# Kernel optimization log

Measured on AMD Instinct MI355X. Metric: run time of the kernel, lower is better.

Reference implementation:

```python
import jax, jax.numpy as jnp
import numpy as np
from jax import lax

NQ = 9          # num_qubits
K = 3           # basis_size
S = 16          # max_num_snapshots
H = 128         # hidden_size
B = 16          # batch
D = 2 ** NQ

# basis_reconstruction buffer = Pauli X, Y, Z (complex64), non-trainable
PAULI = jnp.array([[[0, 1], [1, 0]],
                   [[0, -1j], [1j, 0]],
                   [[1, 0], [0, -1]]], dtype=jnp.complex64)


def setup_inputs() -> dict:
    key = jax.random.key(0)
    ks = jax.random.split(key, 11)
    return {
        "snapshot": jax.random.normal(ks[0], (B, NQ), jnp.float32),
        "basis_comp_vector": jax.random.uniform(ks[1], (B, NQ, K), dtype=jnp.float32),
        "rho": jax.random.normal(ks[2], (B, 2) + (2,) * NQ, jnp.float32),
        "h0": jax.random.normal(ks[3], (B, H), jnp.float32),
        "c0": jax.random.normal(ks[4], (B, H), jnp.float32),
        "W_ih": jax.random.normal(ks[5], (4 * H, NQ + NQ * K), jnp.float32) * 0.1,
        "W_hh": jax.random.normal(ks[6], (4 * H, H), jnp.float32) * 0.1,
        "b_ih": jax.random.normal(ks[7], (4 * H,), jnp.float32) * 0.1,
        "b_hh": jax.random.normal(ks[8], (4 * H,), jnp.float32) * 0.1,
        "Wp": jax.random.normal(ks[9], (NQ, K, H), jnp.float32) * 0.1,
        "bp": jax.random.normal(ks[10], (NQ, K), jnp.float32) * 0.1,
    }


def _lstm_cell(x, h, c, W_ih, W_hh, b_ih, b_hh):
    g = x @ W_ih.T + h @ W_hh.T + b_ih + b_hh
    i, f, gg, o = jnp.split(g, 4, axis=-1)  # torch gate order i,f,g,o
    i, f, o = jax.nn.sigmoid(i), jax.nn.sigmoid(f), jax.nn.sigmoid(o)
    c = f * c + i * jnp.tanh(gg)
    return o * jnp.tanh(c), c


def _apply_1q(psi, M, i):
    """Apply per-batch 2x2 matrix M [B,2,2] to qubit i of psi [B]+[2]*NQ."""
    psi = jnp.moveaxis(psi, 1 + i, 1)
    sh = psi.shape
    out = jnp.einsum('bij,bjr->bir', M, psi.reshape(sh[0], 2, -1))
    return jnp.moveaxis(out.reshape(sh), 1, 1 + i)


def _take_snapshots(psi, a):
    """Vectorized take_snapshot: psi [B]+[2]*NQ complex, a [B,NQ,K] real (sqrt of probs).
    For each qubit build psi_plus/psi_minus projectors, record expectation
    s = <P+> - <P-> and collapse onto the (normalized) plus branch."""
    axs = tuple(range(1, NQ + 1))
    zeros = jnp.zeros(psi.shape[0], jnp.float32)
    ss = []
    for i in range(NQ):
        a1, a2, a3 = a[:, i, 0], a[:, i, 1], a[:, i, 2]
        an = jnp.sqrt(a1 * a1 + a2 * a2 + a3 * a3)
        nrm = 1.0 / jnp.sqrt(2.0 * an * (a3 + an))
        pp = jnp.stack([lax.complex(a3 + an, zeros), lax.complex(a1, a2)], axis=-1) * nrm[:, None]
        pm = jnp.stack([lax.complex(-a1, a2), lax.complex(a3 + an, zeros)], axis=-1) * nrm[:, None]
        Pp = pp[:, :, None] * jnp.conj(pp)[:, None, :]  # [B,2,2]
        Pm = pm[:, :, None] * jnp.conj(pm)[:, None, :]
        psi_p = _apply_1q(psi, Pp, i)
        psi_m = _apply_1q(psi, Pm, i)
        prob_p = jnp.sum(psi_p.real ** 2 + psi_p.imag ** 2, axis=axs)
        prob_m = jnp.sum(psi_m.real ** 2 + psi_m.imag ** 2, axis=axs)
        ss.append(prob_p - prob_m)
        psi = psi_p / jnp.sqrt(prob_p).reshape((-1,) + (1,) * NQ)  # collapse
    return jnp.stack(ss, axis=1)  # [B,NQ]


def _bkron(A, Bm):
    b, m, n = A.shape
    p, q = Bm.shape[1], Bm.shape[2]
    return (A[:, :, None, :, None] * Bm[:, None, :, None, :]).reshape(b, m * p, n * q)


def _forward(snapshot, basis_comp_vector, rho, h0, c0, W_ih, W_hh, b_ih, b_hh, Wp, bp):
    b = snapshot.shape[0]
    psi = lax.complex(rho[:, 0], rho[:, 1])  # [B]+[2]*NQ pure state
    x = jnp.concatenate([snapshot, basis_comp_vector.reshape(b, -1)], axis=-1)
    inputs = [x]
    h, c = h0, c0
    for _ in range(S - 1):
        h, c = _lstm_cell(x, h, c, W_ih, W_hh, b_ih, b_hh)
        probs = jax.nn.softmax(jnp.einsum('bh,nkh->bnk', h, Wp) + bp, axis=-1)
        amps = jnp.sqrt(probs)  # [B,NQ,K]
        snap = _take_snapshots(psi, amps)
        x = jnp.concatenate([snap, amps.reshape(b, -1)], axis=-1)
        inputs.append(x)
    # classical-shadow reconstruction, summed over snapshots
    I2 = jnp.eye(2, dtype=jnp.complex64)
    acc = jnp.zeros((b, D, D), jnp.complex64)
    last_bv = None
    for x in inputs:
        shadow = x[:, :NQ]                                   # [B,NQ]
        bv = x[:, NQ:].reshape(b, NQ, K)
        last_bv = bv
        basis = jnp.einsum('bnk,kij->bnij', bv.astype(jnp.complex64), PAULI)
        rho_q = (I2 + shadow[:, :, None, None].astype(jnp.complex64) * basis * 3.0) / 2.0
        r = rho_q[:, 0]
        for iq in range(1, NQ):
            r = _bkron(r, rho_q[:, iq])
        acc = acc + r
    rho_rec = acc / S
    out = jnp.stack([rho_rec.real, rho_rec.imag], axis=1)  # [B,2,D,D]
    return out, last_bv


def reference(snapshot, basis_comp_vector, rho, h0, c0, W_ih, W_hh, b_ih, b_hh, Wp, bp):
    return _forward(snapshot, basis_comp_vector, rho, h0, c0,
                    W_ih, W_hh, b_ih, b_hh, Wp, bp)
```

## Files before the change

kernel.cpp:

```cpp
#include <hip/hip_runtime.h>
#include <math.h>

#define NQ 9
#define KK 3
#define S 16
#define H 128
#define BB 16
#define D 512
#define DD (D*D)

__device__ __forceinline__ float sigf(float x){ return 1.f/(1.f + __expf(-x)); }

#define DPP_ADD(x, ctrl, rmask) \
  x += __int_as_float(__builtin_amdgcn_update_dpp(0, __float_as_int(x), ctrl, rmask, 0xf, false))

__device__ __forceinline__ float wave_red_sum(float x) {
  DPP_ADD(x, 0x111, 0xf);
  DPP_ADD(x, 0x112, 0xf);
  DPP_ADD(x, 0x114, 0xf);
  DPP_ADD(x, 0x118, 0xf);
  DPP_ADD(x, 0x142, 0xa);
  DPP_ADD(x, 0x143, 0xc);
  return __int_as_float(__builtin_amdgcn_readlane(__float_as_int(x), 63));
}
#define RL(v, l) __int_as_float(__builtin_amdgcn_readlane(__float_as_int(v), (l)))
#define DPP_ROR(x, n) \
  __int_as_float(__builtin_amdgcn_update_dpp(0, __float_as_int(x), 0x120 + (n), 0xf, 0xf, false))

__global__ __launch_bounds__(512, 2)
void seq_kernel(const float* __restrict__ snapshot,
                const float* __restrict__ bcv,
                const float* __restrict__ rho,
                const float* __restrict__ h0,
                const float* __restrict__ c0,
                const float* __restrict__ W_ih,
                const float* __restrict__ W_hh,
                const float* __restrict__ b_ih,
                const float* __restrict__ b_hh,
                const float* __restrict__ Wp,
                const float* __restrict__ bp,
                float4* __restrict__ mats,
                float* __restrict__ last_bv)
{
  const int b    = blockIdx.x;
  const int tid  = threadIdx.x;
  const int lane = tid & 63;
  const int w    = tid >> 6;

  __shared__ __align__(16) float xh[164];
  __shared__ float gbuf[512];
  __shared__ float prj[27];

  float4 wih[9], whh[32];
  {
    const float4* wi = (const float4*)(W_ih + tid*36);
    #pragma unroll
    for (int k = 0; k < 9; ++k) wih[k] = wi[k];
    const float4* wh = (const float4*)(W_hh + tid*H);
    #pragma unroll
    for (int k = 0; k < 32; ++k) whh[k] = wh[k];
  }
  const float bias = b_ih[tid] + b_hh[tid];
  float2 wpv[4]; float bpv[4];
  #pragma unroll
  for (int i = 0; i < 4; ++i) {
    int u = w + 8*i;
    if (u < 27) { wpv[i] = *(const float2*)(Wp + u*H + 2*lane); bpv[i] = bp[u]; }
    else        { wpv[i] = make_float2(0.f, 0.f); bpv[i] = 0.f; }
  }

  float cc0 = c0[b*H + 2*lane], cc1 = c0[b*H + 2*lane + 1];

  float pr0[8], pi0[8], norm0 = 0.f;
  if (w == 0) {
    #pragma unroll
    for (int j = 0; j < 8; ++j) {
      pr0[j] = rho[b*1024 + j*64 + lane];
      pi0[j] = rho[b*1024 + 512 + j*64 + lane];
    }
    float ls = 0.f;
    #pragma unroll
    for (int j = 0; j < 8; ++j) ls += pr0[j]*pr0[j] + pi0[j]*pi0[j];
    norm0 = wave_red_sum(ls);
  }

  if (tid < 128) xh[36 + tid] = h0[b*H + tid];
  if (tid < NQ)  xh[tid]      = snapshot[b*NQ + tid];
  if (tid < 27)  xh[NQ + tid] = bcv[b*27 + tid];
  __syncthreads();

  if (tid < NQ) {
    float s = xh[tid], v0 = xh[9+tid*3], v1 = xh[9+tid*3+1], v2 = xh[9+tid*3+2];
    mats[(b*S + 0)*NQ + tid] = make_float4(
        0.5f*(1.f + 3.f*s*v2), 1.5f*s*v0, -1.5f*s*v1, 0.5f*(1.f - 3.f*s*v2));
  }

  for (int t = 1; t < S; ++t) {
    {
      const float4* x4 = (const float4*)xh;
      float g0 = bias, g1 = 0.f, g2 = 0.f, g3 = 0.f;
      #pragma unroll
      for (int k = 0; k < 9; ++k) {
        float4 wv = wih[k], xv = x4[k];
        g0 += wv.x*xv.x; g1 += wv.y*xv.y; g2 += wv.z*xv.z; g3 += wv.w*xv.w;
      }
      #pragma unroll
      for (int k = 0; k < 32; ++k) {
        float4 wv = whh[k], xv = x4[9 + k];
        g0 += wv.x*xv.x; g1 += wv.y*xv.y; g2 += wv.z*xv.z; g3 += wv.w*xv.w;
      }
      gbuf[tid] = (g0 + g1) + (g2 + g3);
    }
    __syncthreads();

    float h0v, h1v;
    {
      float2 gI = *(const float2*)(gbuf + 2*lane);
      float2 gF = *(const float2*)(gbuf + 128 + 2*lane);
      float2 gG = *(const float2*)(gbuf + 256 + 2*lane);
      float2 gO = *(const float2*)(gbuf + 384 + 2*lane);
      cc0 = sigf(gF.x)*cc0 + sigf(gI.x)*tanhf(gG.x);
      cc1 = sigf(gF.y)*cc1 + sigf(gI.y)*tanhf(gG.y);
      h0v = sigf(gO.x)*tanhf(cc0);
      h1v = sigf(gO.y)*tanhf(cc1);
    }
    if (w == 1) *(float2*)(xh + 36 + 2*lane) = make_float2(h0v, h1v);

    #pragma unroll
    for (int i = 0; i < 4; ++i) {
      float p = wave_red_sum(wpv[i].x*h0v + wpv[i].y*h1v);
      int u = w + 8*i;
      if (u < 27 && lane == 0) prj[u] = p + bpv[i];
    }
    __syncthreads();

    if (w == 0) {
      float a1 = 0.f, a2 = 0.f, a3 = 0.f;
      float k0v = 0.f, k1rv = 0.f, k1iv = 0.f;
      if (lane < NQ) {
        float l0 = prj[lane*3], l1 = prj[lane*3+1], l2 = prj[lane*3+2];
        float mx = fmaxf(l0, fmaxf(l1, l2));
        float e0 = __expf(l0 - mx), e1 = __expf(l1 - mx), e2 = __expf(l2 - mx);
        float inv = 1.f/(e0 + e1 + e2);
        a1 = sqrtf(e0*inv); a2 = sqrtf(e1*inv); a3 = sqrtf(e2*inv);
        float an = sqrtf(a1*a1 + a2*a2 + a3*a3);
        float t3 = a3 + an;
        float n1 = 1.f/sqrtf(2.f*an*t3);
        k0v = n1*t3; k1rv = n1*a1; k1iv = -n1*a2;
      }
      float part[9];

      float r4[4], i4[4];
      {
        const float K0 = RL(k0v,0), K1r = RL(k1rv,0), K1i = RL(k1iv,0);
        float lp = 0.f;
        #pragma unroll
        for (int j = 0; j < 4; ++j) {
          r4[j] = K0*pr0[j] + K1r*pr0[j+4] - K1i*pi0[j+4];
          i4[j] = K0*pi0[j] + K1r*pi0[j+4] + K1i*pr0[j+4];
          lp += r4[j]*r4[j] + i4[j]*i4[j];
        }
        part[0] = lp;
      }
      float r2[2], i2[2];
      {
        const float K0 = RL(k0v,1), K1r = RL(k1rv,1), K1i = RL(k1iv,1);
        float lp = 0.f;
        #pragma unroll
        for (int j = 0; j < 2; ++j) {
          r2[j] = K0*r4[j] + K1r*r4[j+2] - K1i*i4[j+2];
          i2[j] = K0*i4[j] + K1r*i4[j+2] + K1i*r4[j+2];
          lp += r2[j]*r2[j] + i2[j]*i2[j];
        }
        part[1] = lp;
      }
      float wr, wi_;
      {
        const float K0 = RL(k0v,2), K1r = RL(k1rv,2), K1i = RL(k1iv,2);
        wr  = K0*r2[0] + K1r*r2[1] - K1i*i2[1];
        wi_ = K0*i2[0] + K1r*i2[1] + K1i*r2[1];
        part[2] = wr*wr + wi_*wi_;
      }
      #pragma unroll
      for (int q = 3; q < 5; ++q) {
        const int half = 32 >> (q - 3);
        const float K0 = RL(k0v,q), K1r = RL(k1rv,q), K1i = RL(k1iv,q);
        float pr = __shfl(wr,  lane + half, 64);
        float pi = __shfl(wi_, lane + half, 64);
        float nr = K0*wr  + K1r*pr - K1i*pi;
        float ni = K0*wi_ + K1r*pi + K1i*pr;
        wr = nr; wi_ = ni;
        part[q] = (lane < half) ? (nr*nr + ni*ni) : 0.f;
      }
      #pragma unroll
      for (int q = 5; q < NQ; ++q) {
        const int half = 32 >> (q - 3);
        const float K0 = RL(k0v,q), K1r = RL(k1rv,q), K1i = RL(k1iv,q);
        float pr, pi;
        if      (q == 5) { pr = DPP_ROR(wr, 8);  pi = DPP_ROR(wi_, 8);  }
        else if (q == 6) { pr = DPP_ROR(wr, 12); pi = DPP_ROR(wi_, 12); }
        else if (q == 7) { pr = DPP_ROR(wr, 14); pi = DPP_ROR(wi_, 14); }
        else             { pr = DPP_ROR(wr, 15); pi = DPP_ROR(wi_, 15); }
        float nr = K0*wr  + K1r*pr - K1i*pi;
        float ni = K0*wi_ + K1r*pi + K1i*pr;
        wr = nr; wi_ = ni;
        part[q] = (lane < half) ? (nr*nr + ni*ni) : 0.f;
      }
      float L[9];
      #pragma unroll
      for (int q = 0; q < NQ; ++q) L[q] = wave_red_sum(part[q]);
      float sv = 2.f*L[0] - norm0;
      #pragma unroll
      for (int q = 1; q < NQ; ++q) {
        float r = 2.f*L[q]/L[q-1] - 1.f;
        sv = (lane == q) ? r : sv;
      }
      if (lane < NQ) {
        xh[lane] = sv;
        xh[9 + lane*3]     = a1;
        xh[9 + lane*3 + 1] = a2;
        xh[9 + lane*3 + 2] = a3;
        mats[(b*S + t)*NQ + lane] = make_float4(
            0.5f*(1.f + 3.f*sv*a3), 1.5f*sv*a1,
            -1.5f*sv*a2,            0.5f*(1.f - 3.f*sv*a3));
      }
    }
    __syncthreads();
  }

  if (tid < 27) last_bv[b*27 + tid] = xh[9 + tid];
}

__device__ __forceinline__ void herm_entry(float4 m, int rb, int cb, float& er, float& ei) {
  if (rb == 0) { if (cb == 0) { er = m.x; ei = 0.f; } else { er = m.y; ei = m.z; } }
  else         { if (cb == 0) { er = m.y; ei = -m.z; } else { er = m.w; ei = 0.f; } }
}

__global__ __launch_bounds__(512, 2)
void kron_kernel(const float4* __restrict__ mats_g, float* __restrict__ out)
{
  const int b   = blockIdx.y;
  const int bm  = blockIdx.x;
  const int tid = threadIdx.x;
  const int rTp = bm >> 3;
  const int rg  = bm & 7;

  __shared__ float4 matsh[S*NQ];
  __shared__ float2 top[S][2][16];
  __shared__ __align__(16) float2 bot[4][S][32];

  if (tid < S*NQ) matsh[tid] = mats_g[b*S*NQ + tid];
  __syncthreads();

  {
    int t = tid >> 5, rTi = (tid >> 4) & 1, cT = tid & 15;
    int rT = rTp*2 + rTi;
    float re = 1.f, im = 0.f;
    #pragma unroll
    for (int q = 0; q < 4; ++q) {
      int rb = (rT >> (3 - q)) & 1, cb = (cT >> (3 - q)) & 1;
      float er, ei; herm_entry(matsh[t*NQ + q], rb, cb, er, ei);
      float nr = re*er - im*ei; im = re*ei + im*er; re = nr;
    }
    top[t][rTi][cT] = make_float2(re, im);
  }
  {
    int r_ = tid >> 7, t_ = (tid >> 3) & 15, cB0 = (tid & 7) << 2;
    int rB = rg*4 + r_;
    #pragma unroll
    for (int i = 0; i < 4; ++i) {
      int cB = cB0 + i;
      float re = 1.f, im = 0.f;
      #pragma unroll
      for (int q = 0; q < 5; ++q) {
        int rb = (rB >> (4 - q)) & 1, cb = (cB >> (4 - q)) & 1;
        float er, ei; herm_entry(matsh[t_*NQ + 4 + q], rb, cb, er, ei);
        float nr = re*er - im*ei; im = re*ei + im*er; re = nr;
      }
      bot[r_][t_][cB] = make_float2(re, im);
    }
  }
  __syncthreads();

  const int rb = tid >> 7;
  const int c0 = (tid & 127) << 2;
  const int cT = c0 >> 5, cB = c0 & 31;
  float4 a0r = make_float4(0,0,0,0), a0i = make_float4(0,0,0,0);
  float4 a1r = make_float4(0,0,0,0), a1i = make_float4(0,0,0,0);
  #pragma unroll
  for (int t = 0; t < S; ++t) {
    float4 b01 = *(const float4*)&bot[rb][t][cB];
    float4 b23 = *(const float4*)&bot[rb][t][cB + 2];
    float2 tA = top[t][0][cT];
    float2 tB = top[t][1][cT];
    a0r.x += tA.x*b01.x - tA.y*b01.y;  a0i.x += tA.x*b01.y + tA.y*b01.x;
    a0r.y += tA.x*b01.z - tA.y*b01.w;  a0i.y += tA.x*b01.w + tA.y*b01.z;
    a0r.z += tA.x*b23.x - tA.y*b23.y;  a0i.z += tA.x*b23.y + tA.y*b23.x;
    a0r.w += tA.x*b23.z - tA.y*b23.w;  a0i.w += tA.x*b23.w + tA.y*b23.z;
    a1r.x += tB.x*b01.x - tB.y*b01.y;  a1i.x += tB.x*b01.y + tB.y*b01.x;
    a1r.y += tB.x*b01.z - tB.y*b01.w;  a1i.y += tB.x*b01.w + tB.y*b01.z;
    a1r.z += tB.x*b23.x - tB.y*b23.y;  a1i.z += tB.x*b23.y + tB.y*b23.x;
    a1r.w += tB.x*b23.z - tB.y*b23.w;  a1i.w += tB.x*b23.w + tB.y*b23.z;
  }
  const float invS = 1.f/16.f;
  a0r.x*=invS; a0r.y*=invS; a0r.z*=invS; a0r.w*=invS;
  a0i.x*=invS; a0i.y*=invS; a0i.z*=invS; a0i.w*=invS;
  a1r.x*=invS; a1r.y*=invS; a1r.z*=invS; a1r.w*=invS;
  a1i.x*=invS; a1i.y*=invS; a1i.z*=invS; a1i.w*=invS;
  const int rowA = (rTp*2)*32 + rg*4 + rb;
  const int rowB = rowA + 32;
  size_t baseA = ((size_t)b*2)*DD + (size_t)rowA*D + c0;
  size_t baseB = ((size_t)b*2)*DD + (size_t)rowB*D + c0;
  *(float4*)(out + baseA)      = a0r;
  *(float4*)(out + baseA + DD) = a0i;
  *(float4*)(out + baseB)      = a1r;
  *(float4*)(out + baseB + DD) = a1i;
}

extern "C" void kernel_launch(void* const* d_in, const int* in_sizes, int n_in,
                              void* d_out, int out_size, void* d_ws, size_t ws_size,
                              hipStream_t stream) {
  const float* snapshot = (const float*)d_in[0];
  const float* bcv      = (const float*)d_in[1];
  const float* rho      = (const float*)d_in[2];
  const float* h0       = (const float*)d_in[3];
  const float* c0       = (const float*)d_in[4];
  const float* W_ih     = (const float*)d_in[5];
  const float* W_hh     = (const float*)d_in[6];
  const float* b_ih     = (const float*)d_in[7];
  const float* b_hh     = (const float*)d_in[8];
  const float* Wp       = (const float*)d_in[9];
  const float* bp       = (const float*)d_in[10];

  float*  out     = (float*)d_out;
  float4* mats    = (float4*)d_ws;
  float*  last_bv = out + (size_t)BB*2*DD;

  seq_kernel<<<BB, 512, 0, stream>>>(snapshot, bcv, rho, h0, c0,
                                     W_ih, W_hh, b_ih, b_hh, Wp, bp,
                                     mats, last_bv);

  dim3 grid(64, BB);
  kron_kernel<<<grid, 512, 0, stream>>>(mats, out);
}
```

Before: 171.5 us.

## Broadcast hidden state via lane reads and enlarge kron output tile per block

The LSTM recurrent matvec now takes h from registers through cross-lane reads (RL) instead of shared memory. It is computed right after the snapshot step, so one h store and its shared-memory round trip leave the critical path. The kron kernel now computes four top rows per block instead of two, halving the grid and reusing each bottom-factor load across more outputs. This raises register pressure in the kron kernel and reduces the number of blocks available to hide store latency.

```diff
diff --git a/kernel.cpp b/kernel.cpp
--- a/kernel.cpp
+++ b/kernel.cpp
@@ -47,7 +47,7 @@
   const int lane = tid & 63;
   const int w    = tid >> 6;
 
-  __shared__ __align__(16) float xh[164];
+  __shared__ __align__(16) float xh[36];
   __shared__ float gbuf[512];
   __shared__ float prj[27];
 
@@ -70,6 +70,7 @@
   }
 
   float cc0 = c0[b*H + 2*lane], cc1 = c0[b*H + 2*lane + 1];
+  float h0v = h0[b*H + 2*lane], h1v = h0[b*H + 2*lane + 1];
 
   float pr0[8], pi0[8], norm0 = 0.f;
   if (w == 0) {
@@ -84,36 +85,39 @@
     norm0 = wave_red_sum(ls);
   }
 
-  if (tid < 128) xh[36 + tid] = h0[b*H + tid];
   if (tid < NQ)  xh[tid]      = snapshot[b*NQ + tid];
   if (tid < 27)  xh[NQ + tid] = bcv[b*27 + tid];
-  __syncthreads();
-
   if (tid < NQ) {
-    float s = xh[tid], v0 = xh[9+tid*3], v1 = xh[9+tid*3+1], v2 = xh[9+tid*3+2];
+    float s  = snapshot[b*NQ + tid];
+    float v0 = bcv[b*27 + tid*3];
+    float v1 = bcv[b*27 + tid*3 + 1];
+    float v2 = bcv[b*27 + tid*3 + 2];
     mats[(b*S + 0)*NQ + tid] = make_float4(
         0.5f*(1.f + 3.f*s*v2), 1.5f*s*v0, -1.5f*s*v1, 0.5f*(1.f - 3.f*s*v2));
   }
+
+  float ghh = bias;
+  #pragma unroll
+  for (int j = 0; j < 32; ++j) {
+    float4 wv = whh[j];
+    ghh += wv.x*RL(h0v, 2*j)     + wv.y*RL(h1v, 2*j)
+         + wv.z*RL(h0v, 2*j + 1) + wv.w*RL(h1v, 2*j + 1);
+  }
+  __syncthreads();
 
   for (int t = 1; t < S; ++t) {
     {
       const float4* x4 = (const float4*)xh;
-      float g0 = bias, g1 = 0.f, g2 = 0.f, g3 = 0.f;
+      float g0 = ghh, g1 = 0.f, g2 = 0.f, g3 = 0.f;
       #pragma unroll
       for (int k = 0; k < 9; ++k) {
         float4 wv = wih[k], xv = x4[k];
         g0 += wv.x*xv.x; g1 += wv.y*xv.y; g2 += wv.z*xv.z; g3 += wv.w*xv.w;
       }
-      #pragma unroll
-      for (int k = 0; k < 32; ++k) {
-        float4 wv = whh[k], xv = x4[9 + k];
-        g0 += wv.x*xv.x; g1 += wv.y*xv.y; g2 += wv.z*xv.z; g3 += wv.w*xv.w;
-      }
       gbuf[tid] = (g0 + g1) + (g2 + g3);
     }
     __syncthreads();
 
-    float h0v, h1v;
     {
       float2 gI = *(const float2*)(gbuf + 2*lane);
       float2 gF = *(const float2*)(gbuf + 128 + 2*lane);
@@ -124,8 +128,6 @@
       h0v = sigf(gO.x)*tanhf(cc0);
       h1v = sigf(gO.y)*tanhf(cc1);
     }
-    if (w == 1) *(float2*)(xh + 36 + 2*lane) = make_float2(h0v, h1v);
-
     #pragma unroll
     for (int i = 0; i < 4; ++i) {
       float p = wave_red_sum(wpv[i].x*h0v + wpv[i].y*h1v);
@@ -225,6 +227,17 @@
             -1.5f*sv*a2,            0.5f*(1.f - 3.f*sv*a3));
       }
     }
+
+    if (t < S - 1) {
+      float g = bias;
+      #pragma unroll
+      for (int j = 0; j < 32; ++j) {
+        float4 wv = whh[j];
+        g += wv.x*RL(h0v, 2*j)     + wv.y*RL(h1v, 2*j)
+           + wv.z*RL(h0v, 2*j + 1) + wv.w*RL(h1v, 2*j + 1);
+      }
+      ghh = g;
+    }
     __syncthreads();
   }
 
@@ -242,19 +255,20 @@
   const int b   = blockIdx.y;
   const int bm  = blockIdx.x;
   const int tid = threadIdx.x;
-  const int rTp = bm >> 3;
-  const int rg  = bm & 7;
+  const int rTg = bm >> 3;
+  const int rBg = bm & 7;
 
   __shared__ float4 matsh[S*NQ];
-  __shared__ float2 top[S][2][16];
+  __shared__ float2 top[S][4][16];
   __shared__ __align__(16) float2 bot[4][S][32];
 
   if (tid < S*NQ) matsh[tid] = mats_g[b*S*NQ + tid];
   __syncthreads();
 
-  {
-    int t = tid >> 5, rTi = (tid >> 4) & 1, cT = tid & 15;
-    int rT = rTp*2 + rTi;
+  #pragma unroll
+  for (int e = tid; e < 1024; e += 512) {
+    int t = e >> 6, rTi = (e >> 4) & 3, cT = e & 15;
+    int rT = rTg*4 + rTi;
     float re = 1.f, im = 0.f;
     #pragma unroll
     for (int q = 0; q < 4; ++q) {
@@ -265,8 +279,9 @@
     top[t][rTi][cT] = make_float2(re, im);
   }
   {
-    int r_ = tid >> 7, t_ = (tid >> 3) & 15, cB0 = (tid & 7) << 2;
-    int rB = rg*4 + r_;
+    int e0 = tid*4;
+    int r_ = e0 >> 9, t_ = (e0 >> 5) & 15, cB0 = e0 & 31;
+    int rB = rBg*4 + r_;
     #pragma unroll
     for (int i = 0; i < 4; ++i) {
       int cB = cB0 + i;
@@ -285,36 +300,35 @@
   const int rb = tid >> 7;
   const int c0 = (tid & 127) << 2;
   const int cT = c0 >> 5, cB = c0 & 31;
-  float4 a0r = make_float4(0,0,0,0), a0i = make_float4(0,0,0,0);
-  float4 a1r = make_float4(0,0,0,0), a1i = make_float4(0,0,0,0);
+  float4 accr[4], acci[4];
+  #pragma unroll
+  for (int i = 0; i < 4; ++i) {
+    accr[i] = make_float4(0.f,0.f,0.f,0.f);
+    acci[i] = make_float4(0.f,0.f,0.f,0.f);
+  }
   #pragma unroll
   for (int t = 0; t < S; ++t) {
     float4 b01 = *(const float4*)&bot[rb][t][cB];
     float4 b23 = *(const float4*)&bot[rb][t][cB + 2];
-    float2 tA = top[t][0][cT];
-    float2 tB = top[t][1][cT];
-    a0r.x += tA.x*b01.x - tA.y*b01.y;  a0i.x += tA.x*b01.y + tA.y*b01.x;
-    a0r.y += tA.x*b01.z - tA.y*b01.w;  a0i.y += tA.x*b01.w + tA.y*b01.z;
-    a0r.z += tA.x*b23.x - tA.y*b23.y;  a0i.z += tA.x*b23.y + tA.y*b23.x;
-    a0r.w += tA.x*b23.z - tA.y*b23.w;  a0i.w += tA.x*b23.w + tA.y*b23.z;
-    a1r.x += tB.x*b01.x - tB.y*b01.y;  a1i.x += tB.x*b01.y + tB.y*b01.x;
-    a1r.y += tB.x*b01.z - tB.y*b01.w;  a1i.y += tB.x*b01.w + tB.y*b01.z;
-    a1r.z += tB.x*b23.x - tB.y*b23.y;  a1i.z += tB.x*b23.y + tB.y*b23.x;
-    a1r.w += tB.x*b23.z - tB.y*b23.w;  a1i.w += tB.x*b23.w + tB.y*b23.z;
+    #pragma unroll
+    for (int i = 0; i < 4; ++i) {
+      float2 tv = top[t][i][cT];
+      accr[i].x += tv.x*b01.x - tv.y*b01.y;  acci[i].x += tv.x*b01.y + tv.y*b01.x;
+      accr[i].y += tv.x*b01.z - tv.y*b01.w;  acci[i].y += tv.x*b01.w + tv.y*b01.z;
+      accr[i].z += tv.x*b23.x - tv.y*b23.y;  acci[i].z += tv.x*b23.y + tv.y*b23.x;
+      accr[i].w += tv.x*b23.z - tv.y*b23.w;  acci[i].w += tv.x*b23.w + tv.y*b23.z;
+    }
   }
   const float invS = 1.f/16.f;
-  a0r.x*=invS; a0r.y*=invS; a0r.z*=invS; a0r.w*=invS;
-  a0i.x*=invS; a0i.y*=invS; a0i.z*=invS; a0i.w*=invS;
-  a1r.x*=invS; a1r.y*=invS; a1r.z*=invS; a1r.w*=invS;
-  a1i.x*=invS; a1i.y*=invS; a1i.z*=invS; a1i.w*=invS;
-  const int rowA = (rTp*2)*32 + rg*4 + rb;
-  const int rowB = rowA + 32;
-  size_t baseA = ((size_t)b*2)*DD + (size_t)rowA*D + c0;
-  size_t baseB = ((size_t)b*2)*DD + (size_t)rowB*D + c0;
-  *(float4*)(out + baseA)      = a0r;
-  *(float4*)(out + baseA + DD) = a0i;
-  *(float4*)(out + baseB)      = a1r;
-  *(float4*)(out + baseB + DD) = a1i;
+  #pragma unroll
+  for (int i = 0; i < 4; ++i) {
+    accr[i].x*=invS; accr[i].y*=invS; accr[i].z*=invS; accr[i].w*=invS;
+    acci[i].x*=invS; acci[i].y*=invS; acci[i].z*=invS; acci[i].w*=invS;
+    int row = (rTg*4 + i)*32 + rBg*4 + rb;
+    size_t base = ((size_t)b*2)*DD + (size_t)row*D + c0;
+    *(float4*)(out + base)      = accr[i];
+    *(float4*)(out + base + DD) = acci[i];
+  }
 }
 
 extern "C" void kernel_launch(void* const* d_in, const int* in_sizes, int n_in,
@@ -340,6 +354,6 @@
                                      W_ih, W_hh, b_ih, b_hh, Wp, bp,
                                      mats, last_bv);
 
-  dim3 grid(64, BB);
+  dim3 grid(32, BB);
   kron_kernel<<<grid, 512, 0, stream>>>(mats, out);
 }
```

Measured after the change: 159.7 us. 6.9% less time.
